# Optimization experiments

Hardware: AMD Instinct MI355X
Metric: run time of the kernel (lower is better)

Reference implementation:

```python
import jax, jax.numpy as jnp
import numpy as np

B, S, D, H = 4, 2048, 1024, 16
HD = D // H  # head_dim = 64


def setup_inputs() -> dict:
    key = jax.random.key(0)
    ks = jax.random.split(key, 9)
    sc = 1.0 / np.sqrt(D)
    return {
        "x": jax.random.normal(ks[0], (B, S, D), dtype=jnp.float32),
        "Wq": jax.random.normal(ks[1], (D, D), dtype=jnp.float32) * sc,
        "bq": jnp.zeros((D,), dtype=jnp.float32),
        "Wk": jax.random.normal(ks[2], (D, D), dtype=jnp.float32) * sc,
        "bk": jnp.zeros((D,), dtype=jnp.float32),
        "Wv": jax.random.normal(ks[3], (D, D), dtype=jnp.float32) * sc,
        "bv": jnp.zeros((D,), dtype=jnp.float32),
        "Wo": jax.random.normal(ks[4], (D, D), dtype=jnp.float32) * sc,
        "bo": jnp.zeros((D,), dtype=jnp.float32),
    }


def reference(x, Wq, bq, Wk, bk, Wv, bv, Wo, bo):
    # QKV projections (torch Linear: x @ W.T + b), reshape to [B, H, S, HD]
    def proj(W, b):
        return (x @ W.T + b).reshape(B, S, H, HD).transpose(0, 2, 1, 3)

    Q, K, V = proj(Wq, bq), proj(Wk, bk), proj(Wv, bv)
    scores = jnp.einsum("bhqd,bhkd->bhqk", Q, K) / jnp.sqrt(jnp.float32(HD))
    attn = jax.nn.softmax(scores, axis=-1)  # dropout is identity at eval
    ctx = jnp.einsum("bhqk,bhkd->bhqd", attn, V)
    ctx = ctx.transpose(0, 2, 1, 3).reshape(B, S, D)
    out = ctx @ Wo.T + bo
    return out, attn
```

## Files before the change

kernel.cpp:

```cpp
#include <hip/hip_runtime.h>
#include <stdint.h>

#define Mm 8192
#define Dd 1024

typedef unsigned short u16;
typedef __attribute__((ext_vector_type(8))) short bf16x8;
typedef __attribute__((ext_vector_type(4))) float f32x4;
typedef __attribute__((ext_vector_type(4))) u16 u16x4;

__device__ __forceinline__ u16 f2bf(float f) {
  union { float f; uint32_t u; } c; c.f = f;
  uint32_t u = c.u;
  return (u16)((u + 0x7fffu + ((u >> 16) & 1u)) >> 16);
}

__device__ __forceinline__ float EXP2(float x) {
#if __has_builtin(__builtin_amdgcn_exp2f)
  return __builtin_amdgcn_exp2f(x);
#else
  return exp2f(x);
#endif
}

__device__ __forceinline__ float LOG2(float x) {
#if __has_builtin(__builtin_amdgcn_logf)
  return __builtin_amdgcn_logf(x);
#else
  return log2f(x);
#endif
}

__device__ __forceinline__ uint32_t cvtpk(float a, float b) {
  uint32_t r;
  asm("v_cvt_pk_bf16_f32 %0, %1, %2" : "=v"(r) : "v"(a), "v"(b));
  return r;
}

__device__ __forceinline__ void gll16(const void* g, void* l) {
  __builtin_amdgcn_global_load_lds((const __attribute__((address_space(1))) void*)g,
                                   (__attribute__((address_space(3))) void*)l, 16, 0, 0);
}

__global__ void cvt_all(const float* __restrict__ x, const float* __restrict__ wq,
                        const float* __restrict__ wk, const float* __restrict__ wv,
                        const float* __restrict__ wo, u16* __restrict__ out) {
  const int xn4 = 2097152, wn4 = 262144;
  const int total = xn4 + 4 * wn4;
  int i = blockIdx.x * blockDim.x + threadIdx.x;
  int stride = gridDim.x * blockDim.x;
  for (; i < total; i += stride) {
    const float* src; int off;
    if (i < xn4) { src = x; off = i; }
    else {
      int j = i - xn4; int wsel = j >> 18; off = j & (wn4 - 1);
      src = (wsel == 0) ? wq : (wsel == 1) ? wk : (wsel == 2) ? wv : wo;
    }
    float4 v = ((const float4*)src)[off];
    u16x4 o;
    o.x = f2bf(v.x); o.y = f2bf(v.y); o.z = f2bf(v.z); o.w = f2bf(v.w);
    ((u16x4*)out)[i] = o;
  }
}

__global__ __launch_bounds__(256) void gemm_qkv(
    const u16* __restrict__ A, const u16* __restrict__ Wt,
    const float* __restrict__ bq, const float* __restrict__ bk, const float* __restrict__ bv,
    u16* __restrict__ Qo, u16* __restrict__ Ko, u16* __restrict__ Vo, float qscale)
{
  __shared__ u16 As[128 * 32];
  __shared__ u16 Bs[128 * 32];
  const int K = 1024, tiles_n = 24;
  int nwg = 64 * 24;
  int bid = blockIdx.x;
  { int q = nwg >> 3; bid = (bid & 7) * q + (bid >> 3); }
  int tm = bid / tiles_n, tn = bid % tiles_n;
  int tid = threadIdx.x;
  int wid = tid >> 6, lane = tid & 63;
  int wr = wid >> 1, wc = wid & 1;

  f32x4 acc[4][4] = {};
  int a_row = wr * 64 + (lane & 15);
  int b_row = wc * 64 + (lane & 15);
  int frag_k = (lane >> 4) * 8;

  const u16* ga0 = A + (size_t)(tm * 128 + wid * 32 + (lane >> 2)) * K + (lane & 3) * 8;
  const u16* ga1 = ga0 + (size_t)16 * K;
  const u16* gb0 = Wt + (size_t)(tn * 128 + wid * 32 + (lane >> 2)) * K + (lane & 3) * 8;
  const u16* gb1 = gb0 + (size_t)16 * K;
  u16* lA0 = As + wid * 1024;
  u16* lA1 = As + wid * 1024 + 512;
  u16* lB0 = Bs + wid * 1024;
  u16* lB1 = Bs + wid * 1024 + 512;

  for (int kt = 0; kt < K; kt += 32) {
    gll16(ga0 + kt, lA0);
    gll16(ga1 + kt, lA1);
    gll16(gb0 + kt, lB0);
    gll16(gb1 + kt, lB1);
    __syncthreads();
    bf16x8 af[4], bfr[4];
#pragma unroll
    for (int i = 0; i < 4; i++)
      af[i] = *(const bf16x8*)(As + (a_row + i * 16) * 32 + frag_k);
#pragma unroll
    for (int i = 0; i < 4; i++)
      bfr[i] = *(const bf16x8*)(Bs + (b_row + i * 16) * 32 + frag_k);
#pragma unroll
    for (int i = 0; i < 4; i++)
#pragma unroll
      for (int j = 0; j < 4; j++)
        acc[i][j] = __builtin_amdgcn_mfma_f32_16x16x32_bf16(af[i], bfr[j], acc[i][j], 0, 0, 0);
    __syncthreads();
  }

#pragma unroll
  for (int i = 0; i < 4; i++) {
#pragma unroll
    for (int j = 0; j < 4; j++) {
      int col = tn * 128 + wc * 64 + j * 16 + (lane & 15);
      int wsel = col >> 10, c10 = col & 1023;
      int h = c10 >> 6, hd = c10 & 63;
      float bvv = (wsel == 0 ? bq : wsel == 1 ? bk : bv)[c10];
      int row0 = tm * 128 + wr * 64 + i * 16 + (lane >> 4) * 4;
      int b_ = row0 >> 11, s0 = row0 & 2047;
      if (wsel == 2) {
        u16x4 o;
#pragma unroll
        for (int r = 0; r < 4; r++) o[r] = f2bf(acc[i][j][r] + bvv);
        *(u16x4*)&Vo[((size_t)(b_ * 16 + h) * 64 + hd) * 2048 + s0] = o;
      } else {
        u16* dst = (wsel == 0) ? Qo : Ko;
        float sc = (wsel == 0) ? qscale : 1.0f;
#pragma unroll
        for (int r = 0; r < 4; r++)
          dst[(((size_t)(b_ * 16 + h) * 2048 + (s0 + r)) << 6) + hd] = f2bf((acc[i][j][r] + bvv) * sc);
      }
    }
  }
}

__global__ __launch_bounds__(256) void gemm_out(
    const u16* __restrict__ A, const u16* __restrict__ Bt,
    const float* __restrict__ bias, float* __restrict__ out,
    int M, int N, int K)
{
  __shared__ u16 As[128 * 32];
  __shared__ u16 Bs[128 * 32];
  int tiles_n = N >> 7;
  int nwg = (M >> 7) * tiles_n;
  int bid = blockIdx.x;
  { int q = nwg >> 3; bid = (bid & 7) * q + (bid >> 3); }
  int tm = bid / tiles_n, tn = bid % tiles_n;
  int tid = threadIdx.x;
  int wid = tid >> 6, lane = tid & 63;
  int wr = wid >> 1, wc = wid & 1;

  f32x4 acc[4][4] = {};
  int a_row = wr * 64 + (lane & 15);
  int b_row = wc * 64 + (lane & 15);
  int frag_k = (lane >> 4) * 8;

  const u16* ga0 = A + (size_t)(tm * 128 + wid * 32 + (lane >> 2)) * K + (lane & 3) * 8;
  const u16* ga1 = ga0 + (size_t)16 * K;
  const u16* gb0 = Bt + (size_t)(tn * 128 + wid * 32 + (lane >> 2)) * K + (lane & 3) * 8;
  const u16* gb1 = gb0 + (size_t)16 * K;
  u16* lA0 = As + wid * 1024;
  u16* lA1 = As + wid * 1024 + 512;
  u16* lB0 = Bs + wid * 1024;
  u16* lB1 = Bs + wid * 1024 + 512;

  for (int kt = 0; kt < K; kt += 32) {
    gll16(ga0 + kt, lA0);
    gll16(ga1 + kt, lA1);
    gll16(gb0 + kt, lB0);
    gll16(gb1 + kt, lB1);
    __syncthreads();
    bf16x8 af[4], bfr[4];
#pragma unroll
    for (int i = 0; i < 4; i++)
      af[i] = *(const bf16x8*)(As + (a_row + i * 16) * 32 + frag_k);
#pragma unroll
    for (int i = 0; i < 4; i++)
      bfr[i] = *(const bf16x8*)(Bs + (b_row + i * 16) * 32 + frag_k);
#pragma unroll
    for (int i = 0; i < 4; i++)
#pragma unroll
      for (int j = 0; j < 4; j++)
        acc[i][j] = __builtin_amdgcn_mfma_f32_16x16x32_bf16(af[i], bfr[j], acc[i][j], 0, 0, 0);
    __syncthreads();
  }

#pragma unroll
  for (int i = 0; i < 4; i++)
#pragma unroll
    for (int j = 0; j < 4; j++) {
      int col = tn * 128 + wc * 64 + j * 16 + (lane & 15);
      float bv = bias[col];
#pragma unroll
      for (int r = 0; r < 4; r++) {
        int row = tm * 128 + wr * 64 + i * 16 + (lane >> 4) * 4 + r;
        out[(size_t)row * N + col] = acc[i][j][r] + bv;
      }
    }
}

__global__ __launch_bounds__(512, 4) void attn_fused(
    const u16* __restrict__ Qb, const u16* __restrict__ Kb,
    const u16* __restrict__ Vtb, float* __restrict__ attn_out,
    u16* __restrict__ ctxb)
{
  __shared__ u16 Ks[8][4096];
  __shared__ u16 Ps[8192];

  int bid = blockIdx.x;
  int swz = (bid & 7) * 128 + (bid >> 3);
  int bh = swz >> 4, qt = swz & 15;
  int tid = threadIdx.x, w = tid >> 6, lane = tid & 63;
  int g = lane >> 4, l15 = lane & 15;

  const u16* Qg = Qb + ((size_t)bh * 2048 + qt * 128) * 64;
  const u16* Kg = Kb + (size_t)bh * 2048 * 64;
  const u16* Vg = Vtb + (size_t)bh * 64 * 2048;
  float* Ag = attn_out + ((size_t)bh * 2048 + qt * 128) * 2048;

  int qloc = w * 16 + l15;
  bf16x8 aq0 = *(const bf16x8*)(Qg + (size_t)qloc * 64 + g * 8);
  bf16x8 aq1 = *(const bf16x8*)(Qg + (size_t)qloc * 64 + 32 + g * 8);

  int srow = w * 8 + (lane >> 3);
  int schunk = (lane & 7) ^ (lane >> 3);
  const u16* Ksrc = Kg + (size_t)srow * 64 + schunk * 8;
  const u16* Vsrc = Vg + (size_t)srow * 2048 + schunk * 8;

  float ls0 = 0.f, ls1 = 0.f, ls2 = 0.f, ls3 = 0.f;
#pragma unroll
  for (int t = 0; t < 4; t++)
    gll16(Ksrc + (size_t)t * 4096, (char*)Ks[t] + w * 1024);
  for (int o = 0; o < 8; ++o) {
    int gb = (o & 1) << 2;
    if (o < 7) {
#pragma unroll
      for (int t = 0; t < 4; t++)
        gll16(Ksrc + (size_t)(4 * o + 4 + t) * 4096, (char*)Ks[(gb ^ 4) + t] + w * 1024);
      asm volatile("s_waitcnt vmcnt(4)" ::: "memory");
    } else {
      asm volatile("s_waitcnt vmcnt(0)" ::: "memory");
    }
    __builtin_amdgcn_s_barrier();
#pragma unroll
    for (int t4 = 0; t4 < 4; t4++) {
      const char* Kbase = (const char*)Ks[gb + t4];
      f32x4 s[4] = {};
      __builtin_amdgcn_s_setprio(1);
#pragma unroll
      for (int t = 0; t < 4; t++) {
        int kr = t * 16 + l15;
        int x = (kr & 7) << 4;
        bf16x8 k0 = *(const bf16x8*)(Kbase + kr * 128 + ((g * 16) ^ x));
        bf16x8 k1 = *(const bf16x8*)(Kbase + kr * 128 + ((64 + g * 16) ^ x));
        s[t] = __builtin_amdgcn_mfma_f32_16x16x32_bf16(k0, aq0, s[t], 0, 0, 0);
        s[t] = __builtin_amdgcn_mfma_f32_16x16x32_bf16(k1, aq1, s[t], 0, 0, 0);
      }
      __builtin_amdgcn_s_setprio(0);
#pragma unroll
      for (int r = 0; r < 4; r++) {
        ls0 += EXP2(s[0][r]); ls1 += EXP2(s[1][r]);
        ls2 += EXP2(s[2][r]); ls3 += EXP2(s[3][r]);
      }
    }
    asm volatile("" ::: "memory");
    __builtin_amdgcn_s_barrier();
  }
  float lsum = (ls0 + ls1) + (ls2 + ls3);
  lsum += __shfl_xor(lsum, 16);
  lsum += __shfl_xor(lsum, 32);
  float lr2 = -LOG2(lsum);

  f32x4 ctx[4] = {};
  int xq = (qloc & 7) << 4;
  char* Pb = (char*)Ps + qloc * 128;
#pragma unroll
  for (int p = 0; p < 3; p++) {
    gll16(Ksrc + (size_t)p * 4096, (char*)Ks[p] + w * 1024);
    gll16(Vsrc + (size_t)p * 64,  (char*)Ks[4 + p] + w * 1024);
  }
  for (int it = 0; it < 32; ++it) {
    int nx = (it + 3) & 31;
    int nb = (it + 3) & 3;
    gll16(Ksrc + (size_t)nx * 4096, (char*)Ks[nb] + w * 1024);
    gll16(Vsrc + (size_t)nx * 64,  (char*)Ks[4 + nb] + w * 1024);
    if (it == 0)      asm volatile("s_waitcnt vmcnt(6)" ::: "memory");
    else if (it == 1) asm volatile("s_waitcnt vmcnt(10)" ::: "memory");
    else if (it == 2) asm volatile("s_waitcnt vmcnt(14)" ::: "memory");
    else              asm volatile("s_waitcnt vmcnt(18)" ::: "memory");
    __builtin_amdgcn_s_barrier();
    f32x4 s[4] = {};
    const char* Kbase = (const char*)Ks[it & 3];
    const char* Vbase = (const char*)Ks[4 + (it & 3)];
    __builtin_amdgcn_s_setprio(1);
#pragma unroll
    for (int t = 0; t < 4; t++) {
      int kr = t * 16 + l15;
      int x = (kr & 7) << 4;
      bf16x8 k0 = *(const bf16x8*)(Kbase + kr * 128 + ((g * 16) ^ x));
      bf16x8 k1 = *(const bf16x8*)(Kbase + kr * 128 + ((64 + g * 16) ^ x));
      s[t] = __builtin_amdgcn_mfma_f32_16x16x32_bf16(k0, aq0, s[t], 0, 0, 0);
      s[t] = __builtin_amdgcn_mfma_f32_16x16x32_bf16(k1, aq1, s[t], 0, 0, 0);
    }
    __builtin_amdgcn_s_setprio(0);
    float* Arow = Ag + (size_t)qloc * 2048 + it * 64 + g * 4;
#pragma unroll
    for (int t = 0; t < 4; t++) {
      f32x4 p;
#pragma unroll
      for (int r = 0; r < 4; r++) p[r] = EXP2(s[t][r] + lr2);
      __builtin_nontemporal_store(p, (f32x4*)(Arow + t * 16));
      uint2 pk;
      pk.x = cvtpk(p[0], p[1]);
      pk.y = cvtpk(p[2], p[3]);
      *(uint2*)(Pb + ((t * 32 + g * 8) ^ xq)) = pk;
    }
    __builtin_amdgcn_s_setprio(1);
#pragma unroll
    for (int kk = 0; kk < 2; kk++) {
      bf16x8 ap = *(const bf16x8*)(Pb + ((kk * 64 + g * 16) ^ xq));
#pragma unroll
      for (int t = 0; t < 4; t++) {
        int dr = t * 16 + l15;
        bf16x8 bv = *(const bf16x8*)(Vbase + dr * 128 + ((kk * 64 + g * 16) ^ ((dr & 7) << 4)));
        ctx[t] = __builtin_amdgcn_mfma_f32_16x16x32_bf16(ap, bv, ctx[t], 0, 0, 0);
      }
    }
    __builtin_amdgcn_s_setprio(0);
    asm volatile("" ::: "memory");
    __builtin_amdgcn_s_barrier();
  }

  int b_ = bh >> 4, h = bh & 15;
#pragma unroll
  for (int t = 0; t < 4; t++)
#pragma unroll
    for (int r = 0; r < 4; r++) {
      int qg = qt * 128 + w * 16 + g * 4 + r;
      int col = h * 64 + t * 16 + l15;
      ctxb[((size_t)b_ * 2048 + qg) * 1024 + col] = f2bf(ctx[t][r]);
    }
}

extern "C" void kernel_launch(void* const* d_in, const int* in_sizes, int n_in,
                              void* d_out, int out_size, void* d_ws, size_t ws_size,
                              hipStream_t stream) {
  const float* x  = (const float*)d_in[0];
  const float* Wq = (const float*)d_in[1];
  const float* bq = (const float*)d_in[2];
  const float* Wk = (const float*)d_in[3];
  const float* bk = (const float*)d_in[4];
  const float* Wv = (const float*)d_in[5];
  const float* bv = (const float*)d_in[6];
  const float* Wo = (const float*)d_in[7];
  const float* bo = (const float*)d_in[8];

  u16* xb   = (u16*)d_ws;
  u16* Wqb  = xb + (size_t)Mm * Dd;
  u16* Wkb  = Wqb + (size_t)Dd * Dd;
  u16* Wvb  = Wkb + (size_t)Dd * Dd;
  u16* Wob  = Wvb + (size_t)Dd * Dd;
  u16* Qb   = Wob + (size_t)Dd * Dd;
  u16* Kbuf = Qb + (size_t)Mm * Dd;
  u16* Vtb  = Kbuf + (size_t)Mm * Dd;
  u16* ctxb = Vtb + (size_t)Mm * Dd;

  float* out_f = (float*)d_out;
  float* attn_o = out_f + (size_t)Mm * Dd;

  cvt_all<<<2048, 256, 0, stream>>>(x, Wq, Wk, Wv, Wo, xb);

  const float qscale = 0.125f * 1.44269504088896340736f;
  gemm_qkv<<<1536, 256, 0, stream>>>(xb, Wqb, bq, bk, bv, Qb, Kbuf, Vtb, qscale);
  attn_fused<<<1024, 512, 0, stream>>>(Qb, Kbuf, Vtb, attn_o, ctxb);
  gemm_out<<<512, 256, 0, stream>>>(ctxb, Wob, bo, out_f, Mm, Dd, Dd);
}
```

Baseline: 436.6 us.

## Process two KV tiles per barrier pair with double-buffered tile groups

Restructures the second-pass attention loop so it handles K/V tiles in pairs. Each of 16 outer iterations prefetches the next pair of tiles into the alternate half of the 4-slot LDS ring, then computes two tiles between one set of barriers. This halves the number of workgroup barriers and waitcnt points. In exchange the prefetch distance drops from three tiles ahead to one pair ahead, which may expose more global load latency.

After: 456.2 us. +4.5%, slower.

```diff
diff --git a/kernel.cpp b/kernel.cpp
--- a/kernel.cpp
+++ b/kernel.cpp
@@ -281,58 +281,65 @@
   int xq = (qloc & 7) << 4;
   char* Pb = (char*)Ps + qloc * 128;
 #pragma unroll
-  for (int p = 0; p < 3; p++) {
-    gll16(Ksrc + (size_t)p * 4096, (char*)Ks[p] + w * 1024);
-    gll16(Vsrc + (size_t)p * 64,  (char*)Ks[4 + p] + w * 1024);
-  }
-  for (int it = 0; it < 32; ++it) {
-    int nx = (it + 3) & 31;
-    int nb = (it + 3) & 3;
-    gll16(Ksrc + (size_t)nx * 4096, (char*)Ks[nb] + w * 1024);
-    gll16(Vsrc + (size_t)nx * 64,  (char*)Ks[4 + nb] + w * 1024);
-    if (it == 0)      asm volatile("s_waitcnt vmcnt(6)" ::: "memory");
-    else if (it == 1) asm volatile("s_waitcnt vmcnt(10)" ::: "memory");
-    else if (it == 2) asm volatile("s_waitcnt vmcnt(14)" ::: "memory");
-    else              asm volatile("s_waitcnt vmcnt(18)" ::: "memory");
+  for (int t = 0; t < 2; t++) {
+    gll16(Ksrc + (size_t)t * 4096, (char*)Ks[t] + w * 1024);
+    gll16(Vsrc + (size_t)t * 64,  (char*)Ks[4 + t] + w * 1024);
+  }
+  for (int o = 0; o < 16; ++o) {
+    int gb = (o & 1) << 1;
+    if (o < 15) {
+#pragma unroll
+      for (int t = 0; t < 2; t++) {
+        gll16(Ksrc + (size_t)(2 * o + 2 + t) * 4096, (char*)Ks[(gb ^ 2) + t] + w * 1024);
+        gll16(Vsrc + (size_t)(2 * o + 2 + t) * 64,  (char*)Ks[4 + (gb ^ 2) + t] + w * 1024);
+      }
+    }
+    if (o == 0)       asm volatile("s_waitcnt vmcnt(4)" ::: "memory");
+    else if (o < 15)  asm volatile("s_waitcnt vmcnt(12)" ::: "memory");
+    else              asm volatile("s_waitcnt vmcnt(8)" ::: "memory");
     __builtin_amdgcn_s_barrier();
-    f32x4 s[4] = {};
-    const char* Kbase = (const char*)Ks[it & 3];
-    const char* Vbase = (const char*)Ks[4 + (it & 3)];
-    __builtin_amdgcn_s_setprio(1);
-#pragma unroll
-    for (int t = 0; t < 4; t++) {
-      int kr = t * 16 + l15;
-      int x = (kr & 7) << 4;
-      bf16x8 k0 = *(const bf16x8*)(Kbase + kr * 128 + ((g * 16) ^ x));
-      bf16x8 k1 = *(const bf16x8*)(Kbase + kr * 128 + ((64 + g * 16) ^ x));
-      s[t] = __builtin_amdgcn_mfma_f32_16x16x32_bf16(k0, aq0, s[t], 0, 0, 0);
-      s[t] = __builtin_amdgcn_mfma_f32_16x16x32_bf16(k1, aq1, s[t], 0, 0, 0);
-    }
-    __builtin_amdgcn_s_setprio(0);
-    float* Arow = Ag + (size_t)qloc * 2048 + it * 64 + g * 4;
-#pragma unroll
-    for (int t = 0; t < 4; t++) {
-      f32x4 p;
-#pragma unroll
-      for (int r = 0; r < 4; r++) p[r] = EXP2(s[t][r] + lr2);
-      __builtin_nontemporal_store(p, (f32x4*)(Arow + t * 16));
-      uint2 pk;
-      pk.x = cvtpk(p[0], p[1]);
-      pk.y = cvtpk(p[2], p[3]);
-      *(uint2*)(Pb + ((t * 32 + g * 8) ^ xq)) = pk;
-    }
-    __builtin_amdgcn_s_setprio(1);
-#pragma unroll
-    for (int kk = 0; kk < 2; kk++) {
-      bf16x8 ap = *(const bf16x8*)(Pb + ((kk * 64 + g * 16) ^ xq));
+#pragma unroll
+    for (int t2 = 0; t2 < 2; t2++) {
+      int it = 2 * o + t2;
+      const char* Kbase = (const char*)Ks[gb + t2];
+      const char* Vbase = (const char*)Ks[4 + gb + t2];
+      f32x4 s[4] = {};
+      __builtin_amdgcn_s_setprio(1);
 #pragma unroll
       for (int t = 0; t < 4; t++) {
-        int dr = t * 16 + l15;
-        bf16x8 bv = *(const bf16x8*)(Vbase + dr * 128 + ((kk * 64 + g * 16) ^ ((dr & 7) << 4)));
-        ctx[t] = __builtin_amdgcn_mfma_f32_16x16x32_bf16(ap, bv, ctx[t], 0, 0, 0);
-      }
-    }
-    __builtin_amdgcn_s_setprio(0);
+        int kr = t * 16 + l15;
+        int x = (kr & 7) << 4;
+        bf16x8 k0 = *(const bf16x8*)(Kbase + kr * 128 + ((g * 16) ^ x));
+        bf16x8 k1 = *(const bf16x8*)(Kbase + kr * 128 + ((64 + g * 16) ^ x));
+        s[t] = __builtin_amdgcn_mfma_f32_16x16x32_bf16(k0, aq0, s[t], 0, 0, 0);
+        s[t] = __builtin_amdgcn_mfma_f32_16x16x32_bf16(k1, aq1, s[t], 0, 0, 0);
+      }
+      __builtin_amdgcn_s_setprio(0);
+      float* Arow = Ag + (size_t)qloc * 2048 + it * 64 + g * 4;
+#pragma unroll
+      for (int t = 0; t < 4; t++) {
+        f32x4 p;
+#pragma unroll
+        for (int r = 0; r < 4; r++) p[r] = EXP2(s[t][r] + lr2);
+        __builtin_nontemporal_store(p, (f32x4*)(Arow + t * 16));
+        uint2 pk;
+        pk.x = cvtpk(p[0], p[1]);
+        pk.y = cvtpk(p[2], p[3]);
+        *(uint2*)(Pb + ((t * 32 + g * 8) ^ xq)) = pk;
+      }
+      __builtin_amdgcn_s_setprio(1);
+#pragma unroll
+      for (int kk = 0; kk < 2; kk++) {
+        bf16x8 ap = *(const bf16x8*)(Pb + ((kk * 64 + g * 16) ^ xq));
+#pragma unroll
+        for (int t = 0; t < 4; t++) {
+          int dr = t * 16 + l15;
+          bf16x8 bv = *(const bf16x8*)(Vbase + dr * 128 + ((kk * 64 + g * 16) ^ ((dr & 7) << 4)));
+          ctx[t] = __builtin_amdgcn_mfma_f32_16x16x32_bf16(ap, bv, ctx[t], 0, 0, 0);
+        }
+      }
+      __builtin_amdgcn_s_setprio(0);
+    }
     asm volatile("" ::: "memory");
     __builtin_amdgcn_s_barrier();
   }
```

## Triple-buffer LDS tiles in projection GEMMs with async prefetch two ahead

Applied to the files above, without the earlier changes.

Both the QKV and output projection GEMMs move from a single LDS buffer with load-then-sync to a three-stage ring buffer. Global-to-LDS loads are issued two K-tiles ahead, and explicit vmcnt waits plus raw barriers replace __syncthreads. This lets memory latency overlap with MFMA work. It also raises MFMA priority with s_setprio, and it triples LDS use per block, which may reduce occupancy.

Result: no change. 439.7 us (+0.7%).

```diff
diff --git a/kernel.cpp b/kernel.cpp
--- a/kernel.cpp
+++ b/kernel.cpp
@@ -68,8 +68,8 @@
     const float* __restrict__ bq, const float* __restrict__ bk, const float* __restrict__ bv,
     u16* __restrict__ Qo, u16* __restrict__ Ko, u16* __restrict__ Vo, float qscale)
 {
-  __shared__ u16 As[128 * 32];
-  __shared__ u16 Bs[128 * 32];
+  __shared__ u16 As[3][4096];
+  __shared__ u16 Bs[3][4096];
   const int K = 1024, tiles_n = 24;
   int nwg = 64 * 24;
   int bid = blockIdx.x;
@@ -88,30 +88,46 @@
   const u16* ga1 = ga0 + (size_t)16 * K;
   const u16* gb0 = Wt + (size_t)(tn * 128 + wid * 32 + (lane >> 2)) * K + (lane & 3) * 8;
   const u16* gb1 = gb0 + (size_t)16 * K;
-  u16* lA0 = As + wid * 1024;
-  u16* lA1 = As + wid * 1024 + 512;
-  u16* lB0 = Bs + wid * 1024;
-  u16* lB1 = Bs + wid * 1024 + 512;
-
-  for (int kt = 0; kt < K; kt += 32) {
-    gll16(ga0 + kt, lA0);
-    gll16(ga1 + kt, lA1);
-    gll16(gb0 + kt, lB0);
-    gll16(gb1 + kt, lB1);
-    __syncthreads();
+  int lofs = wid * 1024;
+
+#pragma unroll
+  for (int p = 0; p < 2; p++) {
+    gll16(ga0 + p * 32, As[p] + lofs);
+    gll16(ga1 + p * 32, As[p] + lofs + 512);
+    gll16(gb0 + p * 32, Bs[p] + lofs);
+    gll16(gb1 + p * 32, Bs[p] + lofs + 512);
+  }
+  for (int it = 0; it < 32; ++it) {
+    if (it < 30) {
+      int nb = (it + 2) % 3, kt = (it + 2) * 32;
+      gll16(ga0 + kt, As[nb] + lofs);
+      gll16(ga1 + kt, As[nb] + lofs + 512);
+      gll16(gb0 + kt, Bs[nb] + lofs);
+      gll16(gb1 + kt, Bs[nb] + lofs + 512);
+      asm volatile("s_waitcnt vmcnt(8)" ::: "memory");
+    } else if (it == 30) {
+      asm volatile("s_waitcnt vmcnt(4)" ::: "memory");
+    } else {
+      asm volatile("s_waitcnt vmcnt(0)" ::: "memory");
+    }
+    __builtin_amdgcn_s_barrier();
+    int cb = it % 3;
     bf16x8 af[4], bfr[4];
 #pragma unroll
     for (int i = 0; i < 4; i++)
-      af[i] = *(const bf16x8*)(As + (a_row + i * 16) * 32 + frag_k);
-#pragma unroll
-    for (int i = 0; i < 4; i++)
-      bfr[i] = *(const bf16x8*)(Bs + (b_row + i * 16) * 32 + frag_k);
+      af[i] = *(const bf16x8*)(As[cb] + (a_row + i * 16) * 32 + frag_k);
+#pragma unroll
+    for (int i = 0; i < 4; i++)
+      bfr[i] = *(const bf16x8*)(Bs[cb] + (b_row + i * 16) * 32 + frag_k);
+    __builtin_amdgcn_s_setprio(1);
 #pragma unroll
     for (int i = 0; i < 4; i++)
 #pragma unroll
       for (int j = 0; j < 4; j++)
         acc[i][j] = __builtin_amdgcn_mfma_f32_16x16x32_bf16(af[i], bfr[j], acc[i][j], 0, 0, 0);
-    __syncthreads();
+    __builtin_amdgcn_s_setprio(0);
+    asm volatile("" ::: "memory");
+    __builtin_amdgcn_s_barrier();
   }
 
 #pragma unroll
@@ -145,8 +161,8 @@
     const float* __restrict__ bias, float* __restrict__ out,
     int M, int N, int K)
 {
-  __shared__ u16 As[128 * 32];
-  __shared__ u16 Bs[128 * 32];
+  __shared__ u16 As[3][4096];
+  __shared__ u16 Bs[3][4096];
   int tiles_n = N >> 7;
   int nwg = (M >> 7) * tiles_n;
   int bid = blockIdx.x;
@@ -165,30 +181,47 @@
   const u16* ga1 = ga0 + (size_t)16 * K;
   const u16* gb0 = Bt + (size_t)(tn * 128 + wid * 32 + (lane >> 2)) * K + (lane & 3) * 8;
   const u16* gb1 = gb0 + (size_t)16 * K;
-  u16* lA0 = As + wid * 1024;
-  u16* lA1 = As + wid * 1024 + 512;
-  u16* lB0 = Bs + wid * 1024;
-  u16* lB1 = Bs + wid * 1024 + 512;
-
-  for (int kt = 0; kt < K; kt += 32) {
-    gll16(ga0 + kt, lA0);
-    gll16(ga1 + kt, lA1);
-    gll16(gb0 + kt, lB0);
-    gll16(gb1 + kt, lB1);
-    __syncthreads();
+  int lofs = wid * 1024;
+
+#pragma unroll
+  for (int p = 0; p < 2; p++) {
+    gll16(ga0 + p * 32, As[p] + lofs);
+    gll16(ga1 + p * 32, As[p] + lofs + 512);
+    gll16(gb0 + p * 32, Bs[p] + lofs);
+    gll16(gb1 + p * 32, Bs[p] + lofs + 512);
+  }
+  int niter = K >> 5;
+  for (int it = 0; it < niter; ++it) {
+    if (it < niter - 2) {
+      int nb = (it + 2) % 3, kt = (it + 2) * 32;
+      gll16(ga0 + kt, As[nb] + lofs);
+      gll16(ga1 + kt, As[nb] + lofs + 512);
+      gll16(gb0 + kt, Bs[nb] + lofs);
+      gll16(gb1 + kt, Bs[nb] + lofs + 512);
+      asm volatile("s_waitcnt vmcnt(8)" ::: "memory");
+    } else if (it == niter - 2) {
+      asm volatile("s_waitcnt vmcnt(4)" ::: "memory");
+    } else {
+      asm volatile("s_waitcnt vmcnt(0)" ::: "memory");
+    }
+    __builtin_amdgcn_s_barrier();
+    int cb = it % 3;
     bf16x8 af[4], bfr[4];
 #pragma unroll
     for (int i = 0; i < 4; i++)
-      af[i] = *(const bf16x8*)(As + (a_row + i * 16) * 32 + frag_k);
-#pragma unroll
-    for (int i = 0; i < 4; i++)
-      bfr[i] = *(const bf16x8*)(Bs + (b_row + i * 16) * 32 + frag_k);
+      af[i] = *(const bf16x8*)(As[cb] + (a_row + i * 16) * 32 + frag_k);
+#pragma unroll
+    for (int i = 0; i < 4; i++)
+      bfr[i] = *(const bf16x8*)(Bs[cb] + (b_row + i * 16) * 32 + frag_k);
+    __builtin_amdgcn_s_setprio(1);
 #pragma unroll
     for (int i = 0; i < 4; i++)
 #pragma unroll
       for (int j = 0; j < 4; j++)
         acc[i][j] = __builtin_amdgcn_mfma_f32_16x16x32_bf16(af[i], bfr[j], acc[i][j], 0, 0, 0);
-    __syncthreads();
+    __builtin_amdgcn_s_setprio(0);
+    asm volatile("" ::: "memory");
+    __builtin_amdgcn_s_barrier();
   }
 
 #pragma unroll
```
